# Kernel optimization log

Measured on AMD Instinct MI355X. Metric: run time of the kernel, lower is better.

Reference implementation:

```python
import jax, jax.numpy as jnp
import numpy as np
import math

D_MODEL = 512
D_HEAD = 64
N_HEADS = D_MODEL // D_HEAD  # 8
COND = 768
K = 7        # neighborhood kernel size
EPS = 1e-6


def _rope_freqs():
    # RoPE(dim=d_head//2, n_heads): freqs geometric in [pi, 10*pi), shape [n_heads, d_head//4]
    dim = D_HEAD // 2
    n = N_HEADS * dim // 2
    freqs = jnp.exp(jnp.linspace(math.log(math.pi), math.log(10.0 * math.pi), n + 1)[:-1])
    return freqs.reshape(dim // 2, N_HEADS).T  # [nh, d_head//4]


def _rms_norm(x, scale, eps):
    mean_sq = jnp.mean(x * x, axis=-1, keepdims=True)
    return x * (scale * jax.lax.rsqrt(mean_sq + eps))


def _apply_rotary(x, theta):
    # rotate first 2*d dims of head dim, leave the rest untouched
    d = theta.shape[-1]
    x1, x2, rest = x[..., :d], x[..., d:2 * d], x[..., 2 * d:]
    cos, sin = jnp.cos(theta), jnp.sin(theta)
    return jnp.concatenate([x1 * cos - x2 * sin, x2 * cos + x1 * sin, rest], axis=-1)


def _nb_idx(L, k):
    # NATTEN border handling: window shifts (clamps) so every query sees exactly k keys
    i = np.arange(L)
    start = np.clip(i - k // 2, 0, L - k)
    return jnp.asarray(start[:, None] + np.arange(k)[None, :])  # [L, k]


def setup_inputs() -> dict:
    key = jax.random.key(0)
    ks = jax.random.split(key, 7)
    N, H, W = 2, 32, 32
    x = jax.random.normal(ks[0], (N, H, W, D_MODEL), jnp.float32)
    pos = jax.random.uniform(ks[1], (N, H, W, 1), jnp.float32, -1.0, 1.0)
    cond = jax.random.normal(ks[2], (N, COND), jnp.float32)
    w_cond = jax.random.normal(ks[3], (D_MODEL, COND), jnp.float32) * 0.02
    w_qkv = jax.random.normal(ks[4], (3 * D_MODEL, D_MODEL), jnp.float32) * 0.02
    scale = jnp.full((N_HEADS,), 10.0, jnp.float32)
    w_out = jax.random.normal(ks[5], (D_MODEL, D_MODEL), jnp.float32) * 0.02
    return {"x": x, "pos": pos, "cond": cond, "w_cond": w_cond,
            "w_qkv": w_qkv, "scale": scale, "w_out": w_out}


def reference(x, pos, cond, w_cond, w_qkv, scale, w_out):
    N, H, W, C = x.shape
    skip = x
    # AdaRMSNorm: rms_norm(x, linear(cond) + 1)
    norm_scale = cond @ w_cond.T + 1.0                  # [N, C]
    xn = _rms_norm(x, norm_scale[:, None, None, :], EPS)
    # qkv projection -> [3, N, nh, H, W, e]
    qkv = (xn @ w_qkv.T).reshape(N, H, W, 3, N_HEADS, D_HEAD)
    qkv = qkv.transpose(3, 0, 4, 1, 2, 5)
    q, k, v = qkv[0], qkv[1], qkv[2]                    # [N, nh, H, W, e]
    # cosine-sim scaling
    sq = jnp.sqrt(scale)[:, None, None, None]           # [nh,1,1,1]
    q = q * (sq * jax.lax.rsqrt(jnp.sum(q * q, -1, keepdims=True) + 1e-6))
    k = k * (sq * jax.lax.rsqrt(jnp.sum(k * k, -1, keepdims=True) + 1e-6))
    # RoPE
    theta = pos[..., None, :] * _rope_freqs()           # [N,H,W,nh,e/4]
    theta = jnp.moveaxis(theta, -2, -4)                 # [N,nh,H,W,e/4]
    q = _apply_rotary(q, theta)
    k = _apply_rotary(k, theta)
    # 2D neighborhood attention (NATTEN, dilation 1)
    ih, iw = _nb_idx(H, K), _nb_idx(W, K)
    Knb = k[:, :, ih][:, :, :, :, iw]                   # [N,nh,H,K,W,K,e]
    Vnb = v[:, :, ih][:, :, :, :, iw]
    qk = jnp.einsum('ncije,nciajbe->ncijab', q, Knb)    # [N,nh,H,W,K,K]
    a = jax.nn.softmax(qk.reshape(N, N_HEADS, H, W, K * K), axis=-1)
    a = a.reshape(N, N_HEADS, H, W, K, K)
    o = jnp.einsum('ncijab,nciajbe->ncije', a, Vnb)     # [N,nh,H,W,e]
    o = o.transpose(0, 2, 3, 1, 4).reshape(N, H, W, C)
    return o @ w_out.T + skip
```

## Files before the change

kernel.cpp:

```cpp
#include <hip/hip_runtime.h>

typedef unsigned short u16;
typedef unsigned int u32;
typedef __bf16 bf16x8 __attribute__((ext_vector_type(8)));
typedef float f32x4 __attribute__((ext_vector_type(4)));

__device__ __forceinline__ float bf2f(u16 v) {
    union { u32 u; float f; } c; c.u = ((u32)v) << 16; return c.f;
}
__device__ __forceinline__ u16 f2bf(float f) {
    union { float f; u32 u; } c; c.f = f;
    u32 u = c.u + 0x7fffu + ((c.u >> 16) & 1u);
    return (u16)(u >> 16);
}

__global__ __launch_bounds__(256) void setup_kernel(
    const float* __restrict__ cond, const float* __restrict__ w_cond,
    const float* __restrict__ x, float* __restrict__ ns, float* __restrict__ inv)
{
    int lane = threadIdx.x & 63;
    int b = blockIdx.x;
    if (b < 256) {
        int wid = b * 4 + (threadIdx.x >> 6);
        int n = wid >> 9, c = wid & 511;
        const float* cp = cond + n * 768;
        const float* wp = w_cond + (size_t)c * 768;
        float s = 0.f;
        #pragma unroll
        for (int j = 0; j < 12; j++)
            s += cp[lane + j * 64] * wp[lane + j * 64];
        #pragma unroll
        for (int d = 1; d < 64; d <<= 1) s += __shfl_xor(s, d);
        if (lane == 0) ns[wid] = s + 1.f;
    } else {
        int p = (b - 256) * 4 + (threadIdx.x >> 6);
        const float* xp = x + (size_t)p * 512;
        float s = 0.f;
        #pragma unroll
        for (int j = 0; j < 8; j++) { float v = xp[lane + j * 64]; s += v * v; }
        #pragma unroll
        for (int d = 1; d < 64; d <<= 1) s += __shfl_xor(s, d);
        if (lane == 0) inv[p] = rsqrtf(s * (1.f / 512.f) + 1e-6f);
    }
}

__global__ __launch_bounds__(256) void convert_kernel(
    const float* __restrict__ x, const float* __restrict__ ns, const float* __restrict__ inv,
    const float* __restrict__ w_qkv, const float* __restrict__ w_out,
    u16* __restrict__ xn, u16* __restrict__ wqkvb, u16* __restrict__ woutb)
{
    int b = blockIdx.x;
    const float* src; u16* dst; size_t i4;
    bool rms = false;
    if (b < 1024)      { src = x;     dst = xn;    i4 = (size_t)(b)        * 1024 + threadIdx.x * 4; rms = true; }
    else if (b < 1792) { src = w_qkv; dst = wqkvb; i4 = (size_t)(b - 1024) * 1024 + threadIdx.x * 4; }
    else               { src = w_out; dst = woutb; i4 = (size_t)(b - 1792) * 1024 + threadIdx.x * 4; }
    float4 v = *(const float4*)(src + i4);
    if (rms) {
        int p = (int)(i4 >> 9), c = (int)(i4 & 511);
        float iv = inv[p];
        float4 nv = *(const float4*)(ns + (p >> 10) * 512 + c);
        v.x *= nv.x * iv; v.y *= nv.y * iv; v.z *= nv.z * iv; v.w *= nv.w * iv;
    }
    ushort4 o; o.x = f2bf(v.x); o.y = f2bf(v.y); o.z = f2bf(v.z); o.w = f2bf(v.w);
    *(ushort4*)(dst + i4) = o;
}

__global__ __launch_bounds__(256) void gemm_qkv(
    const u16* __restrict__ A, const u16* __restrict__ B,
    const float* __restrict__ pos, const float* __restrict__ scale,
    u16* __restrict__ qp, u16* __restrict__ kp, u16* __restrict__ vp)
{
    __shared__ __align__(16) u16 As[64][40];
    __shared__ __align__(16) u16 Bs[64][40];
    int tid = threadIdx.x;
    int lane = tid & 63;
    int w = tid >> 6;
    int wm = w >> 1, wn = w & 1;
    int bm = blockIdx.x * 64, bn = blockIdx.y * 64;
    int qk = blockIdx.y >> 3, h = blockIdx.y & 7;
    int lrow = tid >> 2, lc8 = (tid & 3) * 8;

    f32x4 zero = {0.f, 0.f, 0.f, 0.f};
    f32x4 acc[2][2];
    acc[0][0] = zero; acc[0][1] = zero; acc[1][0] = zero; acc[1][1] = zero;

    const u16* Ap = A + (size_t)(bm + lrow) * 512 + lc8;
    const u16* Bp = B + (size_t)(bn + lrow) * 512 + lc8;
    int m = lane & 15, quad = lane >> 4, kq = quad * 8;

    for (int k0 = 0; k0 < 512; k0 += 32) {
        *(uint4*)&As[lrow][lc8] = *(const uint4*)(Ap + k0);
        *(uint4*)&Bs[lrow][lc8] = *(const uint4*)(Bp + k0);
        __syncthreads();
        #pragma unroll
        for (int ri = 0; ri < 2; ri++) {
            bf16x8 af = *(const bf16x8*)&As[wm * 32 + ri * 16 + m][kq];
            #pragma unroll
            for (int ci = 0; ci < 2; ci++) {
                bf16x8 bfr = *(const bf16x8*)&Bs[wn * 32 + ci * 16 + m][kq];
                acc[ri][ci] = __builtin_amdgcn_mfma_f32_16x16x32_bf16(af, bfr, acc[ri][ci], 0, 0, 0);
            }
        }
        __syncthreads();
    }

    float invn[2][4];
    if (qk < 2) {
        float* red = (float*)As;
        #pragma unroll
        for (int ri = 0; ri < 2; ri++)
        #pragma unroll
        for (int reg = 0; reg < 4; reg++) {
            float pa = acc[ri][0][reg] * acc[ri][0][reg]
                     + acc[ri][1][reg] * acc[ri][1][reg];
            #pragma unroll
            for (int d = 1; d < 16; d <<= 1) pa += __shfl_xor(pa, d);
            if (m == 0) red[(wm * 32 + ri * 16 + quad * 4 + reg) * 2 + wn] = pa;
        }
        __syncthreads();
        float sq = sqrtf(scale[h]);
        #pragma unroll
        for (int ri = 0; ri < 2; ri++)
        #pragma unroll
        for (int reg = 0; reg < 4; reg++) {
            int rl = wm * 32 + ri * 16 + quad * 4 + reg;
            invn[ri][reg] = sq * rsqrtf(red[rl * 2] + red[rl * 2 + 1] + 1e-6f);
        }
    }
    u16* plane = (qk == 0) ? qp : (qk == 1) ? kp : vp;
    float fr = 3.14159265358979323846f * expf((float)(m * 8 + h) * (2.302585092994046f / 128.f));
    #pragma unroll
    for (int ri = 0; ri < 2; ri++)
    #pragma unroll
    for (int reg = 0; reg < 4; reg++) {
        int rl = wm * 32 + ri * 16 + quad * 4 + reg;
        int p = bm + rl;
        size_t basep = ((size_t)((p >> 10) * 8 + h) * 1024 + (p & 1023)) * 64;
        float v0 = acc[ri][0][reg], v1 = acc[ri][1][reg];
        if (qk < 2) {
            float ivn = invn[ri][reg];
            v0 *= ivn; v1 *= ivn;
            if (wn == 0) {
                float th = pos[p] * fr;
                float cs = cosf(th), sn = sinf(th);
                float o0 = v0 * cs - v1 * sn;
                float o1 = v1 * cs + v0 * sn;
                v0 = o0; v1 = o1;
            }
        }
        plane[basep + wn * 32 + m]      = f2bf(v0);
        plane[basep + wn * 32 + 16 + m] = f2bf(v1);
    }
}

__global__ __launch_bounds__(256) void gemm_out(
    const u16* __restrict__ A, const u16* __restrict__ B,
    float* __restrict__ C, const float* __restrict__ skip, int N, int K)
{
    __shared__ __align__(16) u16 As[64][40];
    __shared__ __align__(16) u16 Bs[64][40];
    int tid = threadIdx.x;
    int lane = tid & 63;
    int w = tid >> 6;
    int wm = w >> 1, wn = w & 1;
    int bm = blockIdx.x * 64, bn = blockIdx.y * 64;
    int lrow = tid >> 2, lc8 = (tid & 3) * 8;

    f32x4 zero = {0.f, 0.f, 0.f, 0.f};
    f32x4 acc[2][2];
    acc[0][0] = zero; acc[0][1] = zero; acc[1][0] = zero; acc[1][1] = zero;

    const u16* Ap = A + (size_t)(bm + lrow) * K + lc8;
    const u16* Bp = B + (size_t)(bn + lrow) * K + lc8;
    int r = lane & 15, kq = (lane >> 4) * 8;

    for (int k0 = 0; k0 < K; k0 += 32) {
        *(uint4*)&As[lrow][lc8] = *(const uint4*)(Ap + k0);
        *(uint4*)&Bs[lrow][lc8] = *(const uint4*)(Bp + k0);
        __syncthreads();
        #pragma unroll
        for (int ri = 0; ri < 2; ri++) {
            bf16x8 af = *(const bf16x8*)&As[wm * 32 + ri * 16 + r][kq];
            #pragma unroll
            for (int ci = 0; ci < 2; ci++) {
                bf16x8 bfr = *(const bf16x8*)&Bs[wn * 32 + ci * 16 + r][kq];
                acc[ri][ci] = __builtin_amdgcn_mfma_f32_16x16x32_bf16(af, bfr, acc[ri][ci], 0, 0, 0);
            }
        }
        __syncthreads();
    }

    #pragma unroll
    for (int ri = 0; ri < 2; ri++)
    #pragma unroll
    for (int ci = 0; ci < 2; ci++) {
        int col = bn + wn * 32 + ci * 16 + (lane & 15);
        int row0 = bm + wm * 32 + ri * 16 + (lane >> 4) * 4;
        #pragma unroll
        for (int reg = 0; reg < 4; reg++) {
            size_t idx = (size_t)(row0 + reg) * N + col;
            C[idx] = acc[ri][ci][reg] + skip[idx];
        }
    }
}

__global__ __launch_bounds__(256) void attn_mfma(
    const u16* __restrict__ qp, const u16* __restrict__ kp, const u16* __restrict__ vp,
    u16* __restrict__ ob)
{
    __shared__ __align__(16) u16 Kb[208 * 72];
    __shared__ __align__(16) u16 Sb[64 * 232];

    int tid = threadIdx.x, lane = tid & 63, w = tid >> 6;
    int bx = blockIdx.x;
    int n = bx >> 7, h = (bx >> 4) & 7, t = bx & 15;
    int ti = (t >> 2) * 8, tj = (t & 3) * 8;
    int r0 = min(max(ti - 3, 0), 18), c0 = min(max(tj - 3, 0), 18);
    const u16* qpl = qp + ((size_t)(n * 8 + h) << 16);
    const u16* kpl = kp + ((size_t)(n * 8 + h) << 16);
    const u16* vpl = vp + ((size_t)(n * 8 + h) << 16);

    for (int g = tid; g < 1568; g += 256) {
        int nb = g >> 3, k8 = (g & 7) << 3;
        int ar = nb / 14, ac = nb - ar * 14;
        *(uint4*)&Kb[nb * 72 + k8] =
            *(const uint4*)&kpl[(size_t)((r0 + ar) * 32 + c0 + ac) * 64 + k8];
    }
    __syncthreads();

    int m = lane & 15, quad = lane >> 4;
    {
        int r = w * 16 + m;
        int tok = (ti + (r >> 3)) * 32 + (tj + (r & 7));
        bf16x8 qf0 = *(const bf16x8*)&qpl[(size_t)tok * 64 + quad * 8];
        bf16x8 qf1 = *(const bf16x8*)&qpl[(size_t)tok * 64 + 32 + quad * 8];
        _Float16* sp = (_Float16*)Sb;
        #pragma unroll
        for (int nt = 0; nt < 13; nt++) {
            f32x4 acc = {0.f, 0.f, 0.f, 0.f};
            bf16x8 b0 = *(const bf16x8*)&Kb[(nt * 16 + m) * 72 + quad * 8];
            bf16x8 b1 = *(const bf16x8*)&Kb[(nt * 16 + m) * 72 + 32 + quad * 8];
            acc = __builtin_amdgcn_mfma_f32_16x16x32_bf16(qf0, b0, acc, 0, 0, 0);
            acc = __builtin_amdgcn_mfma_f32_16x16x32_bf16(qf1, b1, acc, 0, 0, 0);
            #pragma unroll
            for (int reg = 0; reg < 4; reg++)
                sp[(w * 16 + quad * 4 + reg) * 232 + nt * 16 + m] = (_Float16)acc[reg];
        }
    }
    __syncthreads();

    for (int g = tid; g < 1568; g += 256) {
        int nb = g >> 3, k8 = (g & 7) << 3;
        int ar = nb / 14, ac = nb - ar * 14;
        uint4 v4 = *(const uint4*)&vpl[(size_t)((r0 + ar) * 32 + c0 + ac) * 64 + k8];
        u32 uu[4] = {v4.x, v4.y, v4.z, v4.w};
        #pragma unroll
        for (int e = 0; e < 4; e++) {
            Kb[(k8 + 2 * e) * 234 + nb]     = (u16)(uu[e] & 0xffff);
            Kb[(k8 + 2 * e + 1) * 234 + nb] = (u16)(uu[e] >> 16);
        }
    }
    for (int g = tid; g < 1792; g += 256) {
        int d = g / 28, nb = 196 + (g - d * 28);
        Kb[d * 234 + nb] = 0;
    }

    {
        int l16 = lane & 15, g4 = lane >> 4;
        #pragma unroll
        for (int it = 0; it < 4; it++) {
            int rr = w * 16 + it * 4 + g4;
            int i2 = ti + (rr >> 3), j2 = tj + (rr & 7);
            int alo = min(max(i2 - 3, 0), 25) - r0;
            int blo = min(max(j2 - 3, 0), 25) - c0;
            const _Float16* sp = (const _Float16*)&Sb[rr * 232];
            float vals[14];
            float mx = -1e30f;
            #pragma unroll
            for (int c = 0; c < 14; c++) {
                int col = l16 + c * 16;
                float v = -1e30f;
                if (col < 196) {
                    int ar = col / 14, ac = col - ar * 14;
                    if (ar >= alo && ar < alo + 7 && ac >= blo && ac < blo + 7)
                        v = (float)sp[col];
                }
                vals[c] = v; mx = fmaxf(mx, v);
            }
            #pragma unroll
            for (int d = 1; d < 16; d <<= 1) mx = fmaxf(mx, __shfl_xor(mx, d));
            float s = 0.f;
            #pragma unroll
            for (int c = 0; c < 14; c++) {
                float e = (vals[c] > -1e29f) ? expf(vals[c] - mx) : 0.f;
                vals[c] = e; s += e;
            }
            #pragma unroll
            for (int d = 1; d < 16; d <<= 1) s += __shfl_xor(s, d);
            float rs = __frcp_rn(s);
            u16* pp = &Sb[rr * 232];
            #pragma unroll
            for (int c = 0; c < 14; c++)
                pp[l16 + c * 16] = f2bf(vals[c] * rs);
        }
    }
    __syncthreads();

    f32x4 oacc[4];
    #pragma unroll
    for (int nt = 0; nt < 4; nt++) { f32x4 z = {0.f,0.f,0.f,0.f}; oacc[nt] = z; }
    #pragma unroll
    for (int ks = 0; ks < 7; ks++) {
        bf16x8 pa = *(const bf16x8*)&Sb[(w * 16 + m) * 232 + ks * 32 + quad * 8];
        #pragma unroll
        for (int nt = 0; nt < 4; nt++) {
            int ad = (nt * 16 + m) * 234 + ks * 32 + quad * 8;
            union { u32 u[4]; bf16x8 v; } vb;
            vb.u[0] = *(const u32*)&Kb[ad];
            vb.u[1] = *(const u32*)&Kb[ad + 2];
            vb.u[2] = *(const u32*)&Kb[ad + 4];
            vb.u[3] = *(const u32*)&Kb[ad + 6];
            oacc[nt] = __builtin_amdgcn_mfma_f32_16x16x32_bf16(pa, vb.v, oacc[nt], 0, 0, 0);
        }
    }
    #pragma unroll
    for (int nt = 0; nt < 4; nt++) {
        #pragma unroll
        for (int reg = 0; reg < 4; reg++) {
            int rr = w * 16 + quad * 4 + reg;
            int tok = (ti + (rr >> 3)) * 32 + (tj + (rr & 7));
            ob[(size_t)(n * 1024 + tok) * 512 + h * 64 + nt * 16 + m] = f2bf(oacc[nt][reg]);
        }
    }
}

extern "C" void kernel_launch(void* const* d_in, const int* in_sizes, int n_in,
                              void* d_out, int out_size, void* d_ws, size_t ws_size,
                              hipStream_t stream)
{
    const float *x = nullptr, *pos = nullptr, *cond = nullptr, *w_cond = nullptr,
                *w_qkv = nullptr, *scale = nullptr, *w_out = nullptr;
    for (int i = 0; i < n_in; i++) {
        switch (in_sizes[i]) {
            case 1048576: x      = (const float*)d_in[i]; break;
            case 2048:    pos    = (const float*)d_in[i]; break;
            case 1536:    cond   = (const float*)d_in[i]; break;
            case 393216:  w_cond = (const float*)d_in[i]; break;
            case 786432:  w_qkv  = (const float*)d_in[i]; break;
            case 8:       scale  = (const float*)d_in[i]; break;
            case 262144:  w_out  = (const float*)d_in[i]; break;
            default: break;
        }
    }
    float* out = (float*)d_out;

    char* ws = (char*)d_ws;
    float* ns    = (float*)ws;
    float* inv   = (float*)(ws + 4096);
    u16*   xn    = (u16*)(ws + 12288);
    u16*   wqkvb = (u16*)(ws + 12288 + 2097152);
    u16*   woutb = (u16*)(ws + 12288 + 3670016);
    u16*   qp    = (u16*)(ws + 12288 + 4194304);
    u16*   kp    = (u16*)(ws + 12288 + 6291456);
    u16*   vp    = (u16*)(ws + 12288 + 8388608);
    u16*   ob    = (u16*)(ws + 12288 + 10485760);

    setup_kernel<<<768, 256, 0, stream>>>(cond, w_cond, x, ns, inv);
    convert_kernel<<<2048, 256, 0, stream>>>(x, ns, inv, w_qkv, w_out, xn, wqkvb, woutb);
    gemm_qkv<<<dim3(32, 24), 256, 0, stream>>>(xn, wqkvb, pos, scale, qp, kp, vp);
    attn_mfma<<<256, 256, 0, stream>>>(qp, kp, vp, ob);
    gemm_out<<<dim3(32, 8), 256, 0, stream>>>(ob, woutb, out, x, 512, 512);
}
```

Before: 115.2 us.

## Fuse RMS-norm scaling into QKV GEMM A-load and merge weight conversion into setup

```diff
diff --git a/kernel.cpp b/kernel.cpp
--- a/kernel.cpp
+++ b/kernel.cpp
@@ -16,58 +16,49 @@
 
 __global__ __launch_bounds__(256) void setup_kernel(
     const float* __restrict__ cond, const float* __restrict__ w_cond,
-    const float* __restrict__ x, float* __restrict__ ns, float* __restrict__ inv)
-{
-    int lane = threadIdx.x & 63;
+    const float* __restrict__ x, const float* __restrict__ w_qkv,
+    const float* __restrict__ w_out,
+    float* __restrict__ ns, float* __restrict__ inv,
+    u16* __restrict__ wqkvb, u16* __restrict__ woutb)
+{
     int b = blockIdx.x;
-    if (b < 256) {
-        int wid = b * 4 + (threadIdx.x >> 6);
-        int n = wid >> 9, c = wid & 511;
-        const float* cp = cond + n * 768;
-        const float* wp = w_cond + (size_t)c * 768;
-        float s = 0.f;
-        #pragma unroll
-        for (int j = 0; j < 12; j++)
-            s += cp[lane + j * 64] * wp[lane + j * 64];
-        #pragma unroll
-        for (int d = 1; d < 64; d <<= 1) s += __shfl_xor(s, d);
-        if (lane == 0) ns[wid] = s + 1.f;
+    if (b < 768) {
+        int lane = threadIdx.x & 63;
+        if (b < 256) {
+            int wid = b * 4 + (threadIdx.x >> 6);
+            int n = wid >> 9, c = wid & 511;
+            const float* cp = cond + n * 768;
+            const float* wp = w_cond + (size_t)c * 768;
+            float s = 0.f;
+            #pragma unroll
+            for (int j = 0; j < 12; j++)
+                s += cp[lane + j * 64] * wp[lane + j * 64];
+            #pragma unroll
+            for (int d = 1; d < 64; d <<= 1) s += __shfl_xor(s, d);
+            if (lane == 0) ns[wid] = s + 1.f;
+        } else {
+            int p = (b - 256) * 4 + (threadIdx.x >> 6);
+            const float* xp = x + (size_t)p * 512;
+            float s = 0.f;
+            #pragma unroll
+            for (int j = 0; j < 8; j++) { float v = xp[lane + j * 64]; s += v * v; }
+            #pragma unroll
+            for (int d = 1; d < 64; d <<= 1) s += __shfl_xor(s, d);
+            if (lane == 0) inv[p] = rsqrtf(s * (1.f / 512.f) + 1e-6f);
+        }
     } else {
-        int p = (b - 256) * 4 + (threadIdx.x >> 6);
-        const float* xp = x + (size_t)p * 512;
-        float s = 0.f;
-        #pragma unroll
-        for (int j = 0; j < 8; j++) { float v = xp[lane + j * 64]; s += v * v; }
-        #pragma unroll
-        for (int d = 1; d < 64; d <<= 1) s += __shfl_xor(s, d);
-        if (lane == 0) inv[p] = rsqrtf(s * (1.f / 512.f) + 1e-6f);
-    }
-}
-
-__global__ __launch_bounds__(256) void convert_kernel(
+        const float* src; u16* dst; size_t i4;
+        if (b < 1536) { src = w_qkv; dst = wqkvb; i4 = (size_t)(b - 768)  * 1024 + threadIdx.x * 4; }
+        else          { src = w_out; dst = woutb; i4 = (size_t)(b - 1536) * 1024 + threadIdx.x * 4; }
+        float4 v = *(const float4*)(src + i4);
+        ushort4 o; o.x = f2bf(v.x); o.y = f2bf(v.y); o.z = f2bf(v.z); o.w = f2bf(v.w);
+        *(ushort4*)(dst + i4) = o;
+    }
+}
+
+__global__ __launch_bounds__(256) void gemm_qkv(
     const float* __restrict__ x, const float* __restrict__ ns, const float* __restrict__ inv,
-    const float* __restrict__ w_qkv, const float* __restrict__ w_out,
-    u16* __restrict__ xn, u16* __restrict__ wqkvb, u16* __restrict__ woutb)
-{
-    int b = blockIdx.x;
-    const float* src; u16* dst; size_t i4;
-    bool rms = false;
-    if (b < 1024)      { src = x;     dst = xn;    i4 = (size_t)(b)        * 1024 + threadIdx.x * 4; rms = true; }
-    else if (b < 1792) { src = w_qkv; dst = wqkvb; i4 = (size_t)(b - 1024) * 1024 + threadIdx.x * 4; }
-    else               { src = w_out; dst = woutb; i4 = (size_t)(b - 1792) * 1024 + threadIdx.x * 4; }
-    float4 v = *(const float4*)(src + i4);
-    if (rms) {
-        int p = (int)(i4 >> 9), c = (int)(i4 & 511);
-        float iv = inv[p];
-        float4 nv = *(const float4*)(ns + (p >> 10) * 512 + c);
-        v.x *= nv.x * iv; v.y *= nv.y * iv; v.z *= nv.z * iv; v.w *= nv.w * iv;
-    }
-    ushort4 o; o.x = f2bf(v.x); o.y = f2bf(v.y); o.z = f2bf(v.z); o.w = f2bf(v.w);
-    *(ushort4*)(dst + i4) = o;
-}
-
-__global__ __launch_bounds__(256) void gemm_qkv(
-    const u16* __restrict__ A, const u16* __restrict__ B,
+    const u16* __restrict__ B,
     const float* __restrict__ pos, const float* __restrict__ scale,
     u16* __restrict__ qp, u16* __restrict__ kp, u16* __restrict__ vp)
 {
@@ -85,12 +76,24 @@
     f32x4 acc[2][2];
     acc[0][0] = zero; acc[0][1] = zero; acc[1][0] = zero; acc[1][1] = zero;
 
-    const u16* Ap = A + (size_t)(bm + lrow) * 512 + lc8;
-    const u16* Bp = B + (size_t)(bn + lrow) * 512 + lc8;
+    int tr = bm + lrow;
+    float iv = inv[tr];
+    const float* Ax  = x  + (size_t)tr * 512 + lc8;
+    const float* nsr = ns + (tr >> 10) * 512 + lc8;
+    const u16*   Bp  = B  + (size_t)(bn + lrow) * 512 + lc8;
     int m = lane & 15, quad = lane >> 4, kq = quad * 8;
 
     for (int k0 = 0; k0 < 512; k0 += 32) {
-        *(uint4*)&As[lrow][lc8] = *(const uint4*)(Ap + k0);
+        float4 a0 = *(const float4*)(Ax + k0);
+        float4 a1 = *(const float4*)(Ax + k0 + 4);
+        float4 n0 = *(const float4*)(nsr + k0);
+        float4 n1 = *(const float4*)(nsr + k0 + 4);
+        uint4 ap;
+        ap.x = (u32)f2bf(a0.x * n0.x * iv) | ((u32)f2bf(a0.y * n0.y * iv) << 16);
+        ap.y = (u32)f2bf(a0.z * n0.z * iv) | ((u32)f2bf(a0.w * n0.w * iv) << 16);
+        ap.z = (u32)f2bf(a1.x * n1.x * iv) | ((u32)f2bf(a1.y * n1.y * iv) << 16);
+        ap.w = (u32)f2bf(a1.z * n1.z * iv) | ((u32)f2bf(a1.w * n1.w * iv) << 16);
+        *(uint4*)&As[lrow][lc8] = ap;
         *(uint4*)&Bs[lrow][lc8] = *(const uint4*)(Bp + k0);
         __syncthreads();
         #pragma unroll
@@ -358,17 +361,15 @@
     char* ws = (char*)d_ws;
     float* ns    = (float*)ws;
     float* inv   = (float*)(ws + 4096);
-    u16*   xn    = (u16*)(ws + 12288);
-    u16*   wqkvb = (u16*)(ws + 12288 + 2097152);
-    u16*   woutb = (u16*)(ws + 12288 + 3670016);
-    u16*   qp    = (u16*)(ws + 12288 + 4194304);
-    u16*   kp    = (u16*)(ws + 12288 + 6291456);
-    u16*   vp    = (u16*)(ws + 12288 + 8388608);
-    u16*   ob    = (u16*)(ws + 12288 + 10485760);
-
-    setup_kernel<<<768, 256, 0, stream>>>(cond, w_cond, x, ns, inv);
-    convert_kernel<<<2048, 256, 0, stream>>>(x, ns, inv, w_qkv, w_out, xn, wqkvb, woutb);
-    gemm_qkv<<<dim3(32, 24), 256, 0, stream>>>(xn, wqkvb, pos, scale, qp, kp, vp);
+    u16*   wqkvb = (u16*)(ws + 12288);
+    u16*   woutb = (u16*)(ws + 12288 + 1572864);
+    u16*   qp    = (u16*)(ws + 12288 + 2097152);
+    u16*   kp    = (u16*)(ws + 12288 + 4194304);
+    u16*   vp    = (u16*)(ws + 12288 + 6291456);
+    u16*   ob    = (u16*)(ws + 12288 + 8388608);
+
+    setup_kernel<<<1792, 256, 0, stream>>>(cond, w_cond, x, w_qkv, w_out, ns, inv, wqkvb, woutb);
+    gemm_qkv<<<dim3(32, 24), 256, 0, stream>>>(x, ns, inv, wqkvb, pos, scale, qp, kp, vp);
     attn_mfma<<<256, 256, 0, stream>>>(qp, kp, vp, ob);
     gemm_out<<<dim3(32, 8), 256, 0, stream>>>(ob, woutb, out, x, 512, 512);
 }
```

Result: slower. 117.5 us (+2.0%).

## Fuse RMS norm into single pass and widen GEMM K-step to 64

Applied to the files above, without the earlier changes.

```diff
diff --git a/kernel.cpp b/kernel.cpp
--- a/kernel.cpp
+++ b/kernel.cpp
@@ -16,11 +16,12 @@
 
 __global__ __launch_bounds__(256) void setup_kernel(
     const float* __restrict__ cond, const float* __restrict__ w_cond,
-    const float* __restrict__ x, float* __restrict__ ns, float* __restrict__ inv)
-{
-    int lane = threadIdx.x & 63;
+    const float* __restrict__ w_qkv, const float* __restrict__ w_out,
+    float* __restrict__ ns, u16* __restrict__ wqkvb, u16* __restrict__ woutb)
+{
     int b = blockIdx.x;
     if (b < 256) {
+        int lane = threadIdx.x & 63;
         int wid = b * 4 + (threadIdx.x >> 6);
         int n = wid >> 9, c = wid & 511;
         const float* cp = cond + n * 768;
@@ -33,37 +34,39 @@
         for (int d = 1; d < 64; d <<= 1) s += __shfl_xor(s, d);
         if (lane == 0) ns[wid] = s + 1.f;
     } else {
-        int p = (b - 256) * 4 + (threadIdx.x >> 6);
-        const float* xp = x + (size_t)p * 512;
-        float s = 0.f;
-        #pragma unroll
-        for (int j = 0; j < 8; j++) { float v = xp[lane + j * 64]; s += v * v; }
-        #pragma unroll
-        for (int d = 1; d < 64; d <<= 1) s += __shfl_xor(s, d);
-        if (lane == 0) inv[p] = rsqrtf(s * (1.f / 512.f) + 1e-6f);
-    }
-}
-
-__global__ __launch_bounds__(256) void convert_kernel(
-    const float* __restrict__ x, const float* __restrict__ ns, const float* __restrict__ inv,
-    const float* __restrict__ w_qkv, const float* __restrict__ w_out,
-    u16* __restrict__ xn, u16* __restrict__ wqkvb, u16* __restrict__ woutb)
-{
-    int b = blockIdx.x;
-    const float* src; u16* dst; size_t i4;
-    bool rms = false;
-    if (b < 1024)      { src = x;     dst = xn;    i4 = (size_t)(b)        * 1024 + threadIdx.x * 4; rms = true; }
-    else if (b < 1792) { src = w_qkv; dst = wqkvb; i4 = (size_t)(b - 1024) * 1024 + threadIdx.x * 4; }
-    else               { src = w_out; dst = woutb; i4 = (size_t)(b - 1792) * 1024 + threadIdx.x * 4; }
-    float4 v = *(const float4*)(src + i4);
-    if (rms) {
-        int p = (int)(i4 >> 9), c = (int)(i4 & 511);
-        float iv = inv[p];
-        float4 nv = *(const float4*)(ns + (p >> 10) * 512 + c);
-        v.x *= nv.x * iv; v.y *= nv.y * iv; v.z *= nv.z * iv; v.w *= nv.w * iv;
-    }
-    ushort4 o; o.x = f2bf(v.x); o.y = f2bf(v.y); o.z = f2bf(v.z); o.w = f2bf(v.w);
-    *(ushort4*)(dst + i4) = o;
+        const float* src; u16* dst; size_t i4;
+        if (b < 1024) { src = w_qkv; dst = wqkvb; i4 = (size_t)(b - 256)  * 1024 + threadIdx.x * 4; }
+        else          { src = w_out; dst = woutb; i4 = (size_t)(b - 1024) * 1024 + threadIdx.x * 4; }
+        float4 v = *(const float4*)(src + i4);
+        ushort4 o; o.x = f2bf(v.x); o.y = f2bf(v.y); o.z = f2bf(v.z); o.w = f2bf(v.w);
+        *(ushort4*)(dst + i4) = o;
+    }
+}
+
+__global__ __launch_bounds__(256) void rmsxn_kernel(
+    const float* __restrict__ x, const float* __restrict__ ns, u16* __restrict__ xn)
+{
+    int w = threadIdx.x >> 6, lane = threadIdx.x & 63;
+    int p = blockIdx.x * 4 + w;
+    int n = p >> 10;
+    const float* xp = x + (size_t)p * 512;
+    const float* nsp = ns + n * 512;
+    float4 v0 = *(const float4*)(xp + lane * 4);
+    float4 v1 = *(const float4*)(xp + 256 + lane * 4);
+    float ss = v0.x * v0.x + v0.y * v0.y + v0.z * v0.z + v0.w * v0.w
+             + v1.x * v1.x + v1.y * v1.y + v1.z * v1.z + v1.w * v1.w;
+    #pragma unroll
+    for (int d = 1; d < 64; d <<= 1) ss += __shfl_xor(ss, d);
+    float inv = rsqrtf(ss * (1.f / 512.f) + 1e-6f);
+    float4 n0 = *(const float4*)(nsp + lane * 4);
+    float4 n1 = *(const float4*)(nsp + 256 + lane * 4);
+    ushort4 o0, o1;
+    o0.x = f2bf(v0.x * n0.x * inv); o0.y = f2bf(v0.y * n0.y * inv);
+    o0.z = f2bf(v0.z * n0.z * inv); o0.w = f2bf(v0.w * n0.w * inv);
+    o1.x = f2bf(v1.x * n1.x * inv); o1.y = f2bf(v1.y * n1.y * inv);
+    o1.z = f2bf(v1.z * n1.z * inv); o1.w = f2bf(v1.w * n1.w * inv);
+    *(ushort4*)(xn + (size_t)p * 512 + lane * 4) = o0;
+    *(ushort4*)(xn + (size_t)p * 512 + 256 + lane * 4) = o1;
 }
 
 __global__ __launch_bounds__(256) void gemm_qkv(
@@ -71,8 +74,8 @@
     const float* __restrict__ pos, const float* __restrict__ scale,
     u16* __restrict__ qp, u16* __restrict__ kp, u16* __restrict__ vp)
 {
-    __shared__ __align__(16) u16 As[64][40];
-    __shared__ __align__(16) u16 Bs[64][40];
+    __shared__ __align__(16) u16 As[2][64][40];
+    __shared__ __align__(16) u16 Bs[2][64][40];
     int tid = threadIdx.x;
     int lane = tid & 63;
     int w = tid >> 6;
@@ -89,16 +92,20 @@
     const u16* Bp = B + (size_t)(bn + lrow) * 512 + lc8;
     int m = lane & 15, quad = lane >> 4, kq = quad * 8;
 
-    for (int k0 = 0; k0 < 512; k0 += 32) {
-        *(uint4*)&As[lrow][lc8] = *(const uint4*)(Ap + k0);
-        *(uint4*)&Bs[lrow][lc8] = *(const uint4*)(Bp + k0);
-        __syncthreads();
+    for (int k0 = 0; k0 < 512; k0 += 64) {
+        *(uint4*)&As[0][lrow][lc8] = *(const uint4*)(Ap + k0);
+        *(uint4*)&As[1][lrow][lc8] = *(const uint4*)(Ap + k0 + 32);
+        *(uint4*)&Bs[0][lrow][lc8] = *(const uint4*)(Bp + k0);
+        *(uint4*)&Bs[1][lrow][lc8] = *(const uint4*)(Bp + k0 + 32);
+        __syncthreads();
+        #pragma unroll
+        for (int kk = 0; kk < 2; kk++)
         #pragma unroll
         for (int ri = 0; ri < 2; ri++) {
-            bf16x8 af = *(const bf16x8*)&As[wm * 32 + ri * 16 + m][kq];
+            bf16x8 af = *(const bf16x8*)&As[kk][wm * 32 + ri * 16 + m][kq];
             #pragma unroll
             for (int ci = 0; ci < 2; ci++) {
-                bf16x8 bfr = *(const bf16x8*)&Bs[wn * 32 + ci * 16 + m][kq];
+                bf16x8 bfr = *(const bf16x8*)&Bs[kk][wn * 32 + ci * 16 + m][kq];
                 acc[ri][ci] = __builtin_amdgcn_mfma_f32_16x16x32_bf16(af, bfr, acc[ri][ci], 0, 0, 0);
             }
         }
@@ -158,8 +165,8 @@
     const u16* __restrict__ A, const u16* __restrict__ B,
     float* __restrict__ C, const float* __restrict__ skip, int N, int K)
 {
-    __shared__ __align__(16) u16 As[64][40];
-    __shared__ __align__(16) u16 Bs[64][40];
+    __shared__ __align__(16) u16 As[2][64][40];
+    __shared__ __align__(16) u16 Bs[2][64][40];
     int tid = threadIdx.x;
     int lane = tid & 63;
     int w = tid >> 6;
@@ -175,16 +182,20 @@
     const u16* Bp = B + (size_t)(bn + lrow) * K + lc8;
     int r = lane & 15, kq = (lane >> 4) * 8;
 
-    for (int k0 = 0; k0 < K; k0 += 32) {
-        *(uint4*)&As[lrow][lc8] = *(const uint4*)(Ap + k0);
-        *(uint4*)&Bs[lrow][lc8] = *(const uint4*)(Bp + k0);
-        __syncthreads();
+    for (int k0 = 0; k0 < K; k0 += 64) {
+        *(uint4*)&As[0][lrow][lc8] = *(const uint4*)(Ap + k0);
+        *(uint4*)&As[1][lrow][lc8] = *(const uint4*)(Ap + k0 + 32);
+        *(uint4*)&Bs[0][lrow][lc8] = *(const uint4*)(Bp + k0);
+        *(uint4*)&Bs[1][lrow][lc8] = *(const uint4*)(Bp + k0 + 32);
+        __syncthreads();
+        #pragma unroll
+        for (int kk = 0; kk < 2; kk++)
         #pragma unroll
         for (int ri = 0; ri < 2; ri++) {
-            bf16x8 af = *(const bf16x8*)&As[wm * 32 + ri * 16 + r][kq];
+            bf16x8 af = *(const bf16x8*)&As[kk][wm * 32 + ri * 16 + r][kq];
             #pragma unroll
             for (int ci = 0; ci < 2; ci++) {
-                bf16x8 bfr = *(const bf16x8*)&Bs[wn * 32 + ci * 16 + r][kq];
+                bf16x8 bfr = *(const bf16x8*)&Bs[kk][wn * 32 + ci * 16 + r][kq];
                 acc[ri][ci] = __builtin_amdgcn_mfma_f32_16x16x32_bf16(af, bfr, acc[ri][ci], 0, 0, 0);
             }
         }
@@ -357,17 +368,16 @@
 
     char* ws = (char*)d_ws;
     float* ns    = (float*)ws;
-    float* inv   = (float*)(ws + 4096);
-    u16*   xn    = (u16*)(ws + 12288);
-    u16*   wqkvb = (u16*)(ws + 12288 + 2097152);
-    u16*   woutb = (u16*)(ws + 12288 + 3670016);
+    u16*   wqkvb = (u16*)(ws + 12288);
+    u16*   woutb = (u16*)(ws + 12288 + 1572864);
+    u16*   xn    = (u16*)(ws + 12288 + 2097152);
     u16*   qp    = (u16*)(ws + 12288 + 4194304);
     u16*   kp    = (u16*)(ws + 12288 + 6291456);
     u16*   vp    = (u16*)(ws + 12288 + 8388608);
     u16*   ob    = (u16*)(ws + 12288 + 10485760);
 
-    setup_kernel<<<768, 256, 0, stream>>>(cond, w_cond, x, ns, inv);
-    convert_kernel<<<2048, 256, 0, stream>>>(x, ns, inv, w_qkv, w_out, xn, wqkvb, woutb);
+    setup_kernel<<<1280, 256, 0, stream>>>(cond, w_cond, w_qkv, w_out, ns, wqkvb, woutb);
+    rmsxn_kernel<<<512, 256, 0, stream>>>(x, ns, xn);
     gemm_qkv<<<dim3(32, 24), 256, 0, stream>>>(xn, wqkvb, pos, scale, qp, kp, vp);
     attn_mfma<<<256, 256, 0, stream>>>(qp, kp, vp, ob);
     gemm_out<<<dim3(32, 8), 256, 0, stream>>>(ob, woutb, out, x, 512, 512);
```

Measured after the change: 111.6 us. 3.1% less time.
